# Optimization experiments

Measured on AMD Instinct MI355X. Metric: run time of the kernel, lower is better.

## Reference

```python
import jax, jax.numpy as jnp
import numpy as np

NEG_SLOPE = 0.2


def _gat_layer(x, W, a_src, a_dst, b, src, dst, num_nodes, concat):
    """PyG-style GATConv (eval mode, self-loops already in src/dst)."""
    H, D = a_src.shape
    h = (x @ W).reshape(num_nodes, H, D)                      # [N,H,D]
    al_src = jnp.einsum('nhd,hd->nh', h, a_src)               # [N,H]
    al_dst = jnp.einsum('nhd,hd->nh', h, a_dst)               # [N,H]
    e = jax.nn.leaky_relu(al_src[src] + al_dst[dst], NEG_SLOPE)  # [E,H]
    m = jax.ops.segment_max(e, dst, num_segments=num_nodes)      # [N,H]
    ex = jnp.exp(e - m[dst])
    denom = jax.ops.segment_sum(ex, dst, num_segments=num_nodes)
    alpha = ex / jnp.maximum(denom[dst], 1e-16)               # [E,H]
    out = jax.ops.segment_sum(alpha[:, :, None] * h[src], dst,
                              num_segments=num_nodes)         # [N,H,D]
    if concat:
        return out.reshape(num_nodes, H * D) + b
    return out.mean(axis=1) + b


def setup_inputs() -> dict:
    key = jax.random.key(0)
    ks = jax.random.split(key, 10)
    N, E, C_IN = 50000, 800000, 256
    H = 4
    d1, d2 = 64, 32  # hidden_channels [256,128] // heads
    inp = {
        'x': jax.random.normal(ks[0], (N, C_IN), jnp.float32),
        'edge_index': jax.random.randint(ks[1], (2, E), 0, N, jnp.int64),
        'W1': jax.random.normal(ks[2], (C_IN, H * d1), jnp.float32) * 0.06,
        'a_src1': jax.random.normal(ks[3], (H, d1), jnp.float32) * 0.1,
        'a_dst1': jax.random.normal(ks[4], (H, d1), jnp.float32) * 0.1,
        'b1': jax.random.normal(ks[5], (H * d1,), jnp.float32) * 0.02,
        'W2': jax.random.normal(ks[6], (H * d1, H * d2), jnp.float32) * 0.06,
        'a_src2': jax.random.normal(ks[7], (H, d2), jnp.float32) * 0.1,
        'a_dst2': jax.random.normal(ks[8], (H, d2), jnp.float32) * 0.1,
        'b2': jax.random.normal(ks[9], (d2,), jnp.float32) * 0.02,
    }
    return inp


def reference(x, edge_index, W1, a_src1, a_dst1, b1, W2, a_src2, a_dst2, b2):
    N = x.shape[0]
    # GATConv adds self-loops by default
    loops = jnp.arange(N, dtype=edge_index.dtype)
    src = jnp.concatenate([edge_index[0], loops])
    dst = jnp.concatenate([edge_index[1], loops])
    # layer 0: concat=True, then leaky_relu (dropout identity in eval)
    h = _gat_layer(x, W1, a_src1, a_dst1, b1, src, dst, N, concat=True)
    h = jax.nn.leaky_relu(h, NEG_SLOPE)
    # layer 1 (last): concat=False -> mean over heads
    out = _gat_layer(h, W2, a_src2, a_dst2, b2, src, dst, N, concat=False)
    return out
```

## Files before the change

### kernel.cpp

```cpp
#include <hip/hip_runtime.h>
#include <hip/hip_fp16.h>

#define NEG_SLOPE_F 0.2f

typedef __attribute__((ext_vector_type(8))) short bf16x8;
typedef __attribute__((ext_vector_type(4))) float f32x4;

__device__ __forceinline__ float lrelu(float v) { return v > 0.0f ? v : NEG_SLOPE_F * v; }

__device__ __forceinline__ unsigned short f2bf(float f) {
  unsigned int u = __float_as_uint(f);
  u += 0x7FFFu + ((u >> 16) & 1u);
  return (unsigned short)(u >> 16);
}
__device__ __forceinline__ float bf2f(unsigned short s) {
  return __uint_as_float(((unsigned int)s) << 16);
}

__global__ void hist_kernel(const int* __restrict__ dst, int* __restrict__ cnt, int E) {
  for (int i = blockIdx.x * blockDim.x + threadIdx.x; i < E; i += gridDim.x * blockDim.x)
    atomicAdd(&cnt[dst[i]], 1);
}

__global__ void chunk_sum_kernel(const int* __restrict__ cnt, int* __restrict__ bsum, int Nn) {
  __shared__ int sm[256];
  int t = threadIdx.x;
  int i = blockIdx.x * 256 + t;
  sm[t] = (i < Nn) ? cnt[i] : 0;
  __syncthreads();
  for (int off = 128; off > 0; off >>= 1) {
    if (t < off) sm[t] += sm[t + off];
    __syncthreads();
  }
  if (t == 0) bsum[blockIdx.x] = sm[0];
}

__global__ void scan_base_kernel(const int* __restrict__ bsum, int* __restrict__ bbase,
                                 int* __restrict__ offs, int nchunk, int Nn) {
  __shared__ int sm[256];
  int t = threadIdx.x;
  int v = (t < nchunk) ? bsum[t] : 0;
  sm[t] = v;
  __syncthreads();
  for (int off = 1; off < 256; off <<= 1) {
    int x = (t >= off) ? sm[t - off] : 0;
    __syncthreads();
    sm[t] += x;
    __syncthreads();
  }
  if (t < nchunk) bbase[t] = sm[t] - v;
  if (t == 255) offs[Nn] = sm[255];
}

__global__ void chunk_scan_kernel(const int* __restrict__ cnt, const int* __restrict__ bbase,
                                  int* __restrict__ offs, int* __restrict__ cur, int Nn) {
  __shared__ int sm[256];
  int t = threadIdx.x;
  int i = blockIdx.x * 256 + t;
  int v = (i < Nn) ? cnt[i] : 0;
  sm[t] = v;
  __syncthreads();
  for (int off = 1; off < 256; off <<= 1) {
    int x = (t >= off) ? sm[t - off] : 0;
    __syncthreads();
    sm[t] += x;
    __syncthreads();
  }
  if (i < Nn) {
    int ex = bbase[blockIdx.x] + sm[t] - v;
    offs[i] = ex;
    cur[i] = ex;
  }
}

__global__ void scatter_kernel(const int* __restrict__ src, const int* __restrict__ dst,
                               int* __restrict__ cur, int* __restrict__ csr, int E) {
  for (int i = blockIdx.x * blockDim.x + threadIdx.x; i < E; i += gridDim.x * blockDim.x) {
    int p = atomicAdd(&cur[dst[i]], 1);
    csr[p] = src[i];
  }
}

__global__ void split_x_kernel(const float* __restrict__ src, unsigned short* __restrict__ dst,
                               int rows) {
  int total = rows * 64;
  for (int i = blockIdx.x * blockDim.x + threadIdx.x; i < total; i += gridDim.x * blockDim.x) {
    int r = i >> 6, c = (i & 63) * 4;
    float4 v = *(const float4*)(src + (size_t)r * 256 + c);
    short4 hv = make_short4((short)f2bf(v.x), (short)f2bf(v.y),
                            (short)f2bf(v.z), (short)f2bf(v.w));
    *(short4*)(dst + (size_t)r * 256 + c) = hv;
  }
}

__global__ void build_bt_kernel(const float* __restrict__ W, unsigned short* __restrict__ Bt,
                                int N) {
  int total = N * 256;
  for (int i = blockIdx.x * blockDim.x + threadIdx.x; i < total; i += gridDim.x * blockDim.x) {
    int n = i >> 8, k = i & 255;
    float v = W[(size_t)k * N + n];
    unsigned short hi = f2bf(v);
    unsigned short lo = f2bf(v - bf2f(hi));
    Bt[(size_t)n * 512 + k] = hi;
    Bt[(size_t)n * 512 + 256 + k] = lo;
  }
}

template <int DLOG>
__global__ __launch_bounds__(256) void gemm_fused(const unsigned short* __restrict__ A,
                                                  const unsigned short* __restrict__ Bt,
                                                  const float* __restrict__ a_src,
                                                  const float* __restrict__ a_dst,
                                                  __half* __restrict__ Ch,
                                                  float* __restrict__ al_s,
                                                  float* __restrict__ al_d,
                                                  int M, int N) {
  __shared__ unsigned short As[128 * 32];
  __shared__ unsigned short Bs[2 * 128 * 32];
  const int tid = threadIdx.x;
  const int lane = tid & 63;
  const int wave = tid >> 6;
  const int wm = (wave >> 1) * 64;
  const int wn = (wave & 1) * 64;
  const int bm = blockIdx.y * 128;
  const int bn = blockIdx.x * 128;
  const int fr = lane & 15;
  const int q = lane >> 4;
  const int srow = tid >> 2;
  const int sslot = tid & 3;
  f32x4 acc[4][4] = {};
  for (int kt = 0; kt < 8; ++kt) {
    const int kk = kt * 32;
#pragma unroll
    for (int i = 0; i < 2; ++i) {
      int r = i * 64 + srow;
      int sl = sslot ^ (r & 3);
      __builtin_amdgcn_global_load_lds(
          (const __attribute__((address_space(1))) unsigned int*)(A + (size_t)(bm + r) * 256 + kk + sl * 8),
          (__attribute__((address_space(3))) unsigned int*)((char*)As + i * 4096 + wave * 1024),
          16, 0, 0);
    }
#pragma unroll
    for (int pp = 0; pp < 2; ++pp) {
#pragma unroll
      for (int i = 0; i < 2; ++i) {
        int r = i * 64 + srow;
        int sl = sslot ^ (r & 3);
        __builtin_amdgcn_global_load_lds(
            (const __attribute__((address_space(1))) unsigned int*)(Bt + (size_t)(bn + r) * 512 + pp * 256 + kk + sl * 8),
            (__attribute__((address_space(3))) unsigned int*)((char*)Bs + pp * 8192 + i * 4096 + wave * 1024),
            16, 0, 0);
      }
    }
    __syncthreads();
    bf16x8 af[4], bh[4], bl[4];
#pragma unroll
    for (int mi = 0; mi < 4; ++mi) {
      int r = wm + mi * 16 + fr;
      af[mi] = *(const bf16x8*)(As + r * 32 + (q ^ (r & 3)) * 8);
    }
#pragma unroll
    for (int ni = 0; ni < 4; ++ni) {
      int r = wn + ni * 16 + fr;
      bh[ni] = *(const bf16x8*)(Bs + r * 32 + (q ^ (r & 3)) * 8);
      bl[ni] = *(const bf16x8*)(Bs + 4096 + r * 32 + (q ^ (r & 3)) * 8);
    }
#pragma unroll
    for (int mi = 0; mi < 4; ++mi)
#pragma unroll
      for (int ni = 0; ni < 4; ++ni) {
        acc[mi][ni] = __builtin_amdgcn_mfma_f32_16x16x32_bf16(af[mi], bh[ni], acc[mi][ni], 0, 0, 0);
        acc[mi][ni] = __builtin_amdgcn_mfma_f32_16x16x32_bf16(af[mi], bl[ni], acc[mi][ni], 0, 0, 0);
      }
    __syncthreads();
  }
  float asv[4], adv[4];
#pragma unroll
  for (int ni = 0; ni < 4; ++ni) {
    int colg = bn + wn + ni * 16 + fr;
    asv[ni] = a_src[colg];
    adv[ni] = a_dst[colg];
  }
  const int hb = (bn + wn) >> DLOG;
#pragma unroll
  for (int mi = 0; mi < 4; ++mi) {
#pragma unroll
    for (int r = 0; r < 4; ++r) {
      int row = bm + wm + mi * 16 + q * 4 + r;
      float ps0 = 0.f, pd0 = 0.f, ps1 = 0.f, pd1 = 0.f;
#pragma unroll
      for (int ni = 0; ni < 4; ++ni) {
        float v = acc[mi][ni][r];
        if (DLOG == 6 || ni < 2) { ps0 += v * asv[ni]; pd0 += v * adv[ni]; }
        else                     { ps1 += v * asv[ni]; pd1 += v * adv[ni]; }
      }
#pragma unroll
      for (int off = 1; off < 16; off <<= 1) {
        ps0 += __shfl_xor(ps0, off, 64);
        pd0 += __shfl_xor(pd0, off, 64);
        if (DLOG == 5) {
          ps1 += __shfl_xor(ps1, off, 64);
          pd1 += __shfl_xor(pd1, off, 64);
        }
      }
      if (fr == 0 && row < M) {
        al_s[row * 4 + hb] = ps0;
        al_d[row * 4 + hb] = pd0;
        if (DLOG == 5) {
          al_s[row * 4 + hb + 1] = ps1;
          al_d[row * 4 + hb + 1] = pd1;
        }
      }
    }
  }
#pragma unroll
  for (int mi = 0; mi < 4; ++mi) {
#pragma unroll
    for (int ni = 0; ni < 4; ++ni) {
      int col = bn + wn + ni * 16 + fr;
#pragma unroll
      for (int r = 0; r < 4; ++r) {
        int row = bm + wm + mi * 16 + q * 4 + r;
        if (row < M) Ch[(size_t)row * N + col] = __float2half(acc[mi][ni][r]);
      }
    }
  }
}

__device__ __forceinline__ float4 ldh4(const __half* __restrict__ hg, int src, int lane) {
  float2 gv = *(const float2*)(hg + (size_t)src * 256 + lane * 4);
  float2 a = __half22float2(*(__half2*)&gv.x);
  float2 b = __half22float2(*(__half2*)&gv.y);
  return make_float4(a.x, a.y, b.x, b.y);
}

__global__ __launch_bounds__(256) void gat_agg1(const __half* __restrict__ hg,
                                                const float* __restrict__ als,
                                                const float* __restrict__ aldv,
                                                const int* __restrict__ offs,
                                                const int* __restrict__ csr,
                                                const float* __restrict__ b1,
                                                unsigned short* __restrict__ A2, int Nn) {
  int node = blockIdx.x * 4 + (threadIdx.x >> 6);
  if (node >= Nn) return;
  int lane = threadIdx.x & 63;
  int head = lane >> 4;
  float ald = aldv[node * 4 + head];
  float p = __expf(lrelu(als[node * 4 + head] + ald));
  float s = p;
  float4 hv0 = ldh4(hg, node, lane);
  float4 acc = make_float4(p * hv0.x, p * hv0.y, p * hv0.z, p * hv0.w);
  int beg = offs[node], end = offs[node + 1];
  int k = beg;
  for (; k + 3 < end; k += 4) {
    int s0 = csr[k], s1 = csr[k + 1], s2 = csr[k + 2], s3 = csr[k + 3];
    float p0 = __expf(lrelu(als[s0 * 4 + head] + ald));
    float p1 = __expf(lrelu(als[s1 * 4 + head] + ald));
    float p2 = __expf(lrelu(als[s2 * 4 + head] + ald));
    float p3 = __expf(lrelu(als[s3 * 4 + head] + ald));
    float4 h0 = ldh4(hg, s0, lane);
    float4 h1 = ldh4(hg, s1, lane);
    float4 h2 = ldh4(hg, s2, lane);
    float4 h3 = ldh4(hg, s3, lane);
    s += (p0 + p1) + (p2 + p3);
    acc.x += (p0 * h0.x + p1 * h1.x) + (p2 * h2.x + p3 * h3.x);
    acc.y += (p0 * h0.y + p1 * h1.y) + (p2 * h2.y + p3 * h3.y);
    acc.z += (p0 * h0.z + p1 * h1.z) + (p2 * h2.z + p3 * h3.z);
    acc.w += (p0 * h0.w + p1 * h1.w) + (p2 * h2.w + p3 * h3.w);
  }
  for (; k < end; ++k) {
    int src = csr[k];
    float pe = __expf(lrelu(als[src * 4 + head] + ald));
    float4 hv = ldh4(hg, src, lane);
    s += pe;
    acc.x += pe * hv.x;
    acc.y += pe * hv.y;
    acc.z += pe * hv.z;
    acc.w += pe * hv.w;
  }
  float inv = 1.f / s;
  const float4 bb = *(const float4*)(b1 + lane * 4);
  float o0 = lrelu(acc.x * inv + bb.x);
  float o1 = lrelu(acc.y * inv + bb.y);
  float o2 = lrelu(acc.z * inv + bb.z);
  float o3 = lrelu(acc.w * inv + bb.w);
  short4 hv = make_short4((short)f2bf(o0), (short)f2bf(o1),
                          (short)f2bf(o2), (short)f2bf(o3));
  *(short4*)(A2 + (size_t)node * 256 + lane * 4) = hv;
}

__global__ __launch_bounds__(256) void gat_agg2(const __half* __restrict__ hg,
                                                const float* __restrict__ als,
                                                const float* __restrict__ aldv,
                                                const int* __restrict__ offs,
                                                const int* __restrict__ csr,
                                                const float* __restrict__ b2,
                                                float* __restrict__ out, int Nn) {
  int node = blockIdx.x * 4 + (threadIdx.x >> 6);
  if (node >= Nn) return;
  int lane = threadIdx.x & 63;
  int head = lane >> 4;
  float ald = aldv[node * 4 + head];
  float p = __expf(lrelu(als[node * 4 + head] + ald));
  float s = p;
  float2 hv0 = __half22float2(*(const __half2*)(hg + (size_t)node * 128 + lane * 2));
  float2 acc = make_float2(p * hv0.x, p * hv0.y);
  int beg = offs[node], end = offs[node + 1];
  int k = beg;
  for (; k + 3 < end; k += 4) {
    int s0 = csr[k], s1 = csr[k + 1], s2 = csr[k + 2], s3 = csr[k + 3];
    float p0 = __expf(lrelu(als[s0 * 4 + head] + ald));
    float p1 = __expf(lrelu(als[s1 * 4 + head] + ald));
    float p2 = __expf(lrelu(als[s2 * 4 + head] + ald));
    float p3 = __expf(lrelu(als[s3 * 4 + head] + ald));
    float2 h0 = __half22float2(*(const __half2*)(hg + (size_t)s0 * 128 + lane * 2));
    float2 h1 = __half22float2(*(const __half2*)(hg + (size_t)s1 * 128 + lane * 2));
    float2 h2 = __half22float2(*(const __half2*)(hg + (size_t)s2 * 128 + lane * 2));
    float2 h3 = __half22float2(*(const __half2*)(hg + (size_t)s3 * 128 + lane * 2));
    s += (p0 + p1) + (p2 + p3);
    acc.x += (p0 * h0.x + p1 * h1.x) + (p2 * h2.x + p3 * h3.x);
    acc.y += (p0 * h0.y + p1 * h1.y) + (p2 * h2.y + p3 * h3.y);
  }
  for (; k < end; ++k) {
    int src = csr[k];
    float pe = __expf(lrelu(als[src * 4 + head] + ald));
    float2 hv = __half22float2(*(const __half2*)(hg + (size_t)src * 128 + lane * 2));
    s += pe;
    acc.x += pe * hv.x;
    acc.y += pe * hv.y;
  }
  float inv = 1.f / s;
  float vx = acc.x * inv, vy = acc.y * inv;
  vx += __shfl_xor(vx, 16, 64);
  vx += __shfl_xor(vx, 32, 64);
  vy += __shfl_xor(vy, 16, 64);
  vy += __shfl_xor(vy, 32, 64);
  if (lane < 16) {
    float2 o;
    o.x = vx * 0.25f + b2[lane * 2 + 0];
    o.y = vy * 0.25f + b2[lane * 2 + 1];
    *(float2*)(out + (size_t)node * 32 + lane * 2) = o;
  }
}

extern "C" void kernel_launch(void* const* d_in, const int* in_sizes, int n_in,
                              void* d_out, int out_size, void* d_ws, size_t ws_size,
                              hipStream_t stream) {
  const float* x   = (const float*)d_in[0];
  const int*   ei  = (const int*)d_in[1];
  const float* W1  = (const float*)d_in[2];
  const float* as1 = (const float*)d_in[3];
  const float* ad1 = (const float*)d_in[4];
  const float* b1  = (const float*)d_in[5];
  const float* W2  = (const float*)d_in[6];
  const float* as2 = (const float*)d_in[7];
  const float* ad2 = (const float*)d_in[8];
  const float* b2  = (const float*)d_in[9];
  float* out = (float*)d_out;

  const int CIN = 256, HD1 = 256, HD2 = 128;
  const int Nn = in_sizes[0] / CIN;
  const int E  = in_sizes[1] / 2;
  const int Mpad = (Nn + 127) & ~127;
  const int nchunk = (Nn + 255) / 256;

  char* p = (char*)d_ws;
  unsigned short* A12 = (unsigned short*)p; p += (size_t)Mpad * 256 * 2;
  __half* hg = (__half*)p; p += (size_t)Nn * 256 * 2;
  unsigned short* Bt1 = (unsigned short*)p; p += (size_t)256 * 512 * 2;
  unsigned short* Bt2 = (unsigned short*)p; p += (size_t)128 * 512 * 2;
  float* als1 = (float*)p; p += (size_t)Nn * 4 * 4;
  float* ald1 = (float*)p; p += (size_t)Nn * 4 * 4;
  float* als2 = (float*)p; p += (size_t)Nn * 4 * 4;
  float* ald2 = (float*)p; p += (size_t)Nn * 4 * 4;
  int* cnt   = (int*)p; p += (size_t)Nn * 4;
  int* offs  = (int*)p; p += (size_t)(Nn + 1) * 4;
  int* cur   = (int*)p; p += (size_t)Nn * 4;
  int* bsum  = (int*)p; p += (size_t)256 * 4;
  int* bbase = (int*)p; p += (size_t)256 * 4;
  int* csr   = (int*)p; p += (size_t)E * 4;

  const int* esrc = ei;
  const int* edst = ei + E;

  hipMemsetAsync(cnt, 0, (size_t)Nn * sizeof(int), stream);
  hist_kernel<<<2048, 256, 0, stream>>>(edst, cnt, E);
  chunk_sum_kernel<<<nchunk, 256, 0, stream>>>(cnt, bsum, Nn);
  scan_base_kernel<<<1, 256, 0, stream>>>(bsum, bbase, offs, nchunk, Nn);
  chunk_scan_kernel<<<nchunk, 256, 0, stream>>>(cnt, bbase, offs, cur, Nn);
  scatter_kernel<<<2048, 256, 0, stream>>>(esrc, edst, cur, csr, E);

  hipMemsetAsync(A12 + (size_t)Nn * 256, 0, (size_t)(Mpad - Nn) * 256 * 2, stream);
  split_x_kernel<<<2048, 256, 0, stream>>>(x, A12, Nn);
  build_bt_kernel<<<256, 256, 0, stream>>>(W1, Bt1, HD1);
  build_bt_kernel<<<128, 256, 0, stream>>>(W2, Bt2, HD2);

  gemm_fused<6><<<dim3(HD1 / 128, Mpad / 128), 256, 0, stream>>>(
      A12, Bt1, as1, ad1, hg, als1, ald1, Nn, HD1);
  gat_agg1<<<(Nn + 3) / 4, 256, 0, stream>>>(hg, als1, ald1, offs, csr, b1, A12, Nn);

  gemm_fused<5><<<dim3(HD2 / 128, Mpad / 128), 256, 0, stream>>>(
      A12, Bt2, as2, ad2, hg, als2, ald2, Nn, HD2);
  gat_agg2<<<(Nn + 3) / 4, 256, 0, stream>>>(hg, als2, ald2, offs, csr, b2, out, Nn);
}
```

Measured before the change: 281.1 us.

## Use half-wave per node in GAT aggregation with wider loads, fuse prep launches

```diff
diff --git a/kernel.cpp b/kernel.cpp
--- a/kernel.cpp
+++ b/kernel.cpp
@@ -82,27 +82,42 @@
 }
 
 __global__ void split_x_kernel(const float* __restrict__ src, unsigned short* __restrict__ dst,
-                               int rows) {
-  int total = rows * 64;
+                               int rows, int rowsPad) {
+  int total = rowsPad * 64;
   for (int i = blockIdx.x * blockDim.x + threadIdx.x; i < total; i += gridDim.x * blockDim.x) {
     int r = i >> 6, c = (i & 63) * 4;
-    float4 v = *(const float4*)(src + (size_t)r * 256 + c);
-    short4 hv = make_short4((short)f2bf(v.x), (short)f2bf(v.y),
-                            (short)f2bf(v.z), (short)f2bf(v.w));
+    short4 hv;
+    if (r < rows) {
+      float4 v = *(const float4*)(src + (size_t)r * 256 + c);
+      hv = make_short4((short)f2bf(v.x), (short)f2bf(v.y),
+                       (short)f2bf(v.z), (short)f2bf(v.w));
+    } else {
+      hv = make_short4(0, 0, 0, 0);
+    }
     *(short4*)(dst + (size_t)r * 256 + c) = hv;
   }
 }
 
-__global__ void build_bt_kernel(const float* __restrict__ W, unsigned short* __restrict__ Bt,
-                                int N) {
-  int total = N * 256;
-  for (int i = blockIdx.x * blockDim.x + threadIdx.x; i < total; i += gridDim.x * blockDim.x) {
+__global__ void build_bt_kernel(const float* __restrict__ W1, const float* __restrict__ W2,
+                                unsigned short* __restrict__ Bt1, unsigned short* __restrict__ Bt2) {
+  int i = blockIdx.x * blockDim.x + threadIdx.x;
+  const int total1 = 256 * 256;
+  const int total2 = 128 * 256;
+  if (i < total1) {
     int n = i >> 8, k = i & 255;
-    float v = W[(size_t)k * N + n];
+    float v = W1[(size_t)k * 256 + n];
     unsigned short hi = f2bf(v);
     unsigned short lo = f2bf(v - bf2f(hi));
-    Bt[(size_t)n * 512 + k] = hi;
-    Bt[(size_t)n * 512 + 256 + k] = lo;
+    Bt1[(size_t)n * 512 + k] = hi;
+    Bt1[(size_t)n * 512 + 256 + k] = lo;
+  } else if (i < total1 + total2) {
+    int j = i - total1;
+    int n = j >> 8, k = j & 255;
+    float v = W2[(size_t)k * 128 + n];
+    unsigned short hi = f2bf(v);
+    unsigned short lo = f2bf(v - bf2f(hi));
+    Bt2[(size_t)n * 512 + k] = hi;
+    Bt2[(size_t)n * 512 + 256 + k] = lo;
   }
 }
 
@@ -227,13 +242,6 @@
   }
 }
 
-__device__ __forceinline__ float4 ldh4(const __half* __restrict__ hg, int src, int lane) {
-  float2 gv = *(const float2*)(hg + (size_t)src * 256 + lane * 4);
-  float2 a = __half22float2(*(__half2*)&gv.x);
-  float2 b = __half22float2(*(__half2*)&gv.y);
-  return make_float4(a.x, a.y, b.x, b.y);
-}
-
 __global__ __launch_bounds__(256) void gat_agg1(const __half* __restrict__ hg,
                                                 const float* __restrict__ als,
                                                 const float* __restrict__ aldv,
@@ -241,15 +249,24 @@
                                                 const int* __restrict__ csr,
                                                 const float* __restrict__ b1,
                                                 unsigned short* __restrict__ A2, int Nn) {
-  int node = blockIdx.x * 4 + (threadIdx.x >> 6);
+  int node = blockIdx.x * 8 + (threadIdx.x >> 5);
   if (node >= Nn) return;
-  int lane = threadIdx.x & 63;
-  int head = lane >> 4;
+  int l = threadIdx.x & 31;
+  int head = l >> 3;
   float ald = aldv[node * 4 + head];
   float p = __expf(lrelu(als[node * 4 + head] + ald));
   float s = p;
-  float4 hv0 = ldh4(hg, node, lane);
-  float4 acc = make_float4(p * hv0.x, p * hv0.y, p * hv0.z, p * hv0.w);
+  float acc[8];
+  {
+    float4 raw = *(const float4*)(hg + (size_t)node * 256 + l * 8);
+    const __half2* hp = (const __half2*)&raw;
+#pragma unroll
+    for (int i = 0; i < 4; ++i) {
+      float2 f = __half22float2(hp[i]);
+      acc[2 * i] = p * f.x;
+      acc[2 * i + 1] = p * f.y;
+    }
+  }
   int beg = offs[node], end = offs[node + 1];
   int k = beg;
   for (; k + 3 < end; k += 4) {
@@ -258,35 +275,51 @@
     float p1 = __expf(lrelu(als[s1 * 4 + head] + ald));
     float p2 = __expf(lrelu(als[s2 * 4 + head] + ald));
     float p3 = __expf(lrelu(als[s3 * 4 + head] + ald));
-    float4 h0 = ldh4(hg, s0, lane);
-    float4 h1 = ldh4(hg, s1, lane);
-    float4 h2 = ldh4(hg, s2, lane);
-    float4 h3 = ldh4(hg, s3, lane);
+    float4 r0 = *(const float4*)(hg + (size_t)s0 * 256 + l * 8);
+    float4 r1 = *(const float4*)(hg + (size_t)s1 * 256 + l * 8);
+    float4 r2 = *(const float4*)(hg + (size_t)s2 * 256 + l * 8);
+    float4 r3 = *(const float4*)(hg + (size_t)s3 * 256 + l * 8);
     s += (p0 + p1) + (p2 + p3);
-    acc.x += (p0 * h0.x + p1 * h1.x) + (p2 * h2.x + p3 * h3.x);
-    acc.y += (p0 * h0.y + p1 * h1.y) + (p2 * h2.y + p3 * h3.y);
-    acc.z += (p0 * h0.z + p1 * h1.z) + (p2 * h2.z + p3 * h3.z);
-    acc.w += (p0 * h0.w + p1 * h1.w) + (p2 * h2.w + p3 * h3.w);
+    const __half2* h0 = (const __half2*)&r0;
+    const __half2* h1 = (const __half2*)&r1;
+    const __half2* h2 = (const __half2*)&r2;
+    const __half2* h3 = (const __half2*)&r3;
+#pragma unroll
+    for (int i = 0; i < 4; ++i) {
+      float2 f0 = __half22float2(h0[i]), f1 = __half22float2(h1[i]);
+      float2 f2 = __half22float2(h2[i]), f3 = __half22float2(h3[i]);
+      acc[2 * i]     += (p0 * f0.x + p1 * f1.x) + (p2 * f2.x + p3 * f3.x);
+      acc[2 * i + 1] += (p0 * f0.y + p1 * f1.y) + (p2 * f2.y + p3 * f3.y);
+    }
   }
   for (; k < end; ++k) {
     int src = csr[k];
     float pe = __expf(lrelu(als[src * 4 + head] + ald));
-    float4 hv = ldh4(hg, src, lane);
+    float4 r0 = *(const float4*)(hg + (size_t)src * 256 + l * 8);
+    const __half2* h0 = (const __half2*)&r0;
     s += pe;
-    acc.x += pe * hv.x;
-    acc.y += pe * hv.y;
-    acc.z += pe * hv.z;
-    acc.w += pe * hv.w;
+#pragma unroll
+    for (int i = 0; i < 4; ++i) {
+      float2 f = __half22float2(h0[i]);
+      acc[2 * i] += pe * f.x;
+      acc[2 * i + 1] += pe * f.y;
+    }
   }
   float inv = 1.f / s;
-  const float4 bb = *(const float4*)(b1 + lane * 4);
-  float o0 = lrelu(acc.x * inv + bb.x);
-  float o1 = lrelu(acc.y * inv + bb.y);
-  float o2 = lrelu(acc.z * inv + bb.z);
-  float o3 = lrelu(acc.w * inv + bb.w);
-  short4 hv = make_short4((short)f2bf(o0), (short)f2bf(o1),
-                          (short)f2bf(o2), (short)f2bf(o3));
-  *(short4*)(A2 + (size_t)node * 256 + lane * 4) = hv;
+  float4 bb0 = *(const float4*)(b1 + l * 8);
+  float4 bb1 = *(const float4*)(b1 + l * 8 + 4);
+  const float* bp = &bb0.x;
+  unsigned short o[8];
+#pragma unroll
+  for (int i = 0; i < 8; ++i) {
+    float b = (i < 4) ? (&bb0.x)[i] : (&bb1.x)[i - 4];
+    o[i] = f2bf(lrelu(acc[i] * inv + b));
+  }
+  (void)bp;
+  short4 w0 = make_short4((short)o[0], (short)o[1], (short)o[2], (short)o[3]);
+  short4 w1 = make_short4((short)o[4], (short)o[5], (short)o[6], (short)o[7]);
+  *(short4*)(A2 + (size_t)node * 256 + l * 8) = w0;
+  *(short4*)(A2 + (size_t)node * 256 + l * 8 + 4) = w1;
 }
 
 __global__ __launch_bounds__(256) void gat_agg2(const __half* __restrict__ hg,
@@ -296,15 +329,24 @@
                                                 const int* __restrict__ csr,
                                                 const float* __restrict__ b2,
                                                 float* __restrict__ out, int Nn) {
-  int node = blockIdx.x * 4 + (threadIdx.x >> 6);
+  int node = blockIdx.x * 8 + (threadIdx.x >> 5);
   if (node >= Nn) return;
-  int lane = threadIdx.x & 63;
-  int head = lane >> 4;
+  int l = threadIdx.x & 31;
+  int head = l >> 3;
   float ald = aldv[node * 4 + head];
   float p = __expf(lrelu(als[node * 4 + head] + ald));
   float s = p;
-  float2 hv0 = __half22float2(*(const __half2*)(hg + (size_t)node * 128 + lane * 2));
-  float2 acc = make_float2(p * hv0.x, p * hv0.y);
+  float acc[4];
+  {
+    float2 raw = *(const float2*)(hg + (size_t)node * 128 + l * 4);
+    const __half2* hp = (const __half2*)&raw;
+#pragma unroll
+    for (int i = 0; i < 2; ++i) {
+      float2 f = __half22float2(hp[i]);
+      acc[2 * i] = p * f.x;
+      acc[2 * i + 1] = p * f.y;
+    }
+  }
   int beg = offs[node], end = offs[node + 1];
   int k = beg;
   for (; k + 3 < end; k += 4) {
@@ -313,33 +355,50 @@
     float p1 = __expf(lrelu(als[s1 * 4 + head] + ald));
     float p2 = __expf(lrelu(als[s2 * 4 + head] + ald));
     float p3 = __expf(lrelu(als[s3 * 4 + head] + ald));
-    float2 h0 = __half22float2(*(const __half2*)(hg + (size_t)s0 * 128 + lane * 2));
-    float2 h1 = __half22float2(*(const __half2*)(hg + (size_t)s1 * 128 + lane * 2));
-    float2 h2 = __half22float2(*(const __half2*)(hg + (size_t)s2 * 128 + lane * 2));
-    float2 h3 = __half22float2(*(const __half2*)(hg + (size_t)s3 * 128 + lane * 2));
+    float2 r0 = *(const float2*)(hg + (size_t)s0 * 128 + l * 4);
+    float2 r1 = *(const float2*)(hg + (size_t)s1 * 128 + l * 4);
+    float2 r2 = *(const float2*)(hg + (size_t)s2 * 128 + l * 4);
+    float2 r3 = *(const float2*)(hg + (size_t)s3 * 128 + l * 4);
     s += (p0 + p1) + (p2 + p3);
-    acc.x += (p0 * h0.x + p1 * h1.x) + (p2 * h2.x + p3 * h3.x);
-    acc.y += (p0 * h0.y + p1 * h1.y) + (p2 * h2.y + p3 * h3.y);
+    const __half2* h0 = (const __half2*)&r0;
+    const __half2* h1 = (const __half2*)&r1;
+    const __half2* h2 = (const __half2*)&r2;
+    const __half2* h3 = (const __half2*)&r3;
+#pragma unroll
+    for (int i = 0; i < 2; ++i) {
+      float2 f0 = __half22float2(h0[i]), f1 = __half22float2(h1[i]);
+      float2 f2 = __half22float2(h2[i]), f3 = __half22float2(h3[i]);
+      acc[2 * i]     += (p0 * f0.x + p1 * f1.x) + (p2 * f2.x + p3 * f3.x);
+      acc[2 * i + 1] += (p0 * f0.y + p1 * f1.y) + (p2 * f2.y + p3 * f3.y);
+    }
   }
   for (; k < end; ++k) {
     int src = csr[k];
     float pe = __expf(lrelu(als[src * 4 + head] + ald));
-    float2 hv = __half22float2(*(const __half2*)(hg + (size_t)src * 128 + lane * 2));
+    float2 r0 = *(const float2*)(hg + (size_t)src * 128 + l * 4);
+    const __half2* h0 = (const __half2*)&r0;
     s += pe;
-    acc.x += pe * hv.x;
-    acc.y += pe * hv.y;
+#pragma unroll
+    for (int i = 0; i < 2; ++i) {
+      float2 f = __half22float2(h0[i]);
+      acc[2 * i] += pe * f.x;
+      acc[2 * i + 1] += pe * f.y;
+    }
   }
   float inv = 1.f / s;
-  float vx = acc.x * inv, vy = acc.y * inv;
-  vx += __shfl_xor(vx, 16, 64);
-  vx += __shfl_xor(vx, 32, 64);
-  vy += __shfl_xor(vy, 16, 64);
-  vy += __shfl_xor(vy, 32, 64);
-  if (lane < 16) {
-    float2 o;
-    o.x = vx * 0.25f + b2[lane * 2 + 0];
-    o.y = vy * 0.25f + b2[lane * 2 + 1];
-    *(float2*)(out + (size_t)node * 32 + lane * 2) = o;
+  float v0 = acc[0] * inv, v1 = acc[1] * inv, v2 = acc[2] * inv, v3 = acc[3] * inv;
+  v0 += __shfl_xor(v0, 8, 64);  v0 += __shfl_xor(v0, 16, 64);
+  v1 += __shfl_xor(v1, 8, 64);  v1 += __shfl_xor(v1, 16, 64);
+  v2 += __shfl_xor(v2, 8, 64);  v2 += __shfl_xor(v2, 16, 64);
+  v3 += __shfl_xor(v3, 8, 64);  v3 += __shfl_xor(v3, 16, 64);
+  if (head == 0) {
+    float4 bb = *(const float4*)(b2 + l * 4);
+    float4 o;
+    o.x = v0 * 0.25f + bb.x;
+    o.y = v1 * 0.25f + bb.y;
+    o.z = v2 * 0.25f + bb.z;
+    o.w = v3 * 0.25f + bb.w;
+    *(float4*)(out + (size_t)node * 32 + l * 4) = o;
   }
 }
 
@@ -390,16 +449,14 @@
   chunk_scan_kernel<<<nchunk, 256, 0, stream>>>(cnt, bbase, offs, cur, Nn);
   scatter_kernel<<<2048, 256, 0, stream>>>(esrc, edst, cur, csr, E);
 
-  hipMemsetAsync(A12 + (size_t)Nn * 256, 0, (size_t)(Mpad - Nn) * 256 * 2, stream);
-  split_x_kernel<<<2048, 256, 0, stream>>>(x, A12, Nn);
-  build_bt_kernel<<<256, 256, 0, stream>>>(W1, Bt1, HD1);
-  build_bt_kernel<<<128, 256, 0, stream>>>(W2, Bt2, HD2);
+  split_x_kernel<<<2048, 256, 0, stream>>>(x, A12, Nn, Mpad);
+  build_bt_kernel<<<384, 256, 0, stream>>>(W1, W2, Bt1, Bt2);
 
   gemm_fused<6><<<dim3(HD1 / 128, Mpad / 128), 256, 0, stream>>>(
       A12, Bt1, as1, ad1, hg, als1, ald1, Nn, HD1);
-  gat_agg1<<<(Nn + 3) / 4, 256, 0, stream>>>(hg, als1, ald1, offs, csr, b1, A12, Nn);
+  gat_agg1<<<(Nn + 7) / 8, 256, 0, stream>>>(hg, als1, ald1, offs, csr, b1, A12, Nn);
 
   gemm_fused<5><<<dim3(HD2 / 128, Mpad / 128), 256, 0, stream>>>(
       A12, Bt2, as2, ad2, hg, als2, ald2, Nn, HD2);
-  gat_agg2<<<(Nn + 3) / 4, 256, 0, stream>>>(hg, als2, ald2, offs, csr, b2, out, Nn);
-}
+  gat_agg2<<<(Nn + 7) / 8, 256, 0, stream>>>(hg, als2, ald2, offs, csr, b2, out, Nn);
+}
```

New measurement: 268.6 us. 1.05x faster.
